# Performance work log

Measured on AMD Instinct MI355X. Metric: run time of the kernel, lower is better.

## Reference

```python
import jax, jax.numpy as jnp
import numpy as np

B, L, H, V = 256, 4096, 64, 64
LN_EPS = 1e-5


def setup_inputs() -> dict:
    key = jax.random.key(0)
    ks = jax.random.split(key, 12)
    s = 1.0 / np.sqrt(H)
    return {
        "seq": jax.random.randint(ks[0], (B, L), 0, V),
        "embed_W": jax.random.normal(ks[1], (V, H), jnp.float32),
        "ff_w1": jax.random.normal(ks[2], (H, 2 * H), jnp.float32) * s,
        "ff_b1": jnp.zeros((2 * H,), jnp.float32),
        "ff_w2": jax.random.normal(ks[3], (2 * H, H), jnp.float32) * s,
        "ff_b2": jnp.zeros((H,), jnp.float32),
        "ln_w": jnp.ones((H,), jnp.float32),
        "ln_b": jnp.zeros((H,), jnp.float32),
        "read_w": jax.random.normal(ks[4], (H, H), jnp.float32) * s,
        "read_b": jnp.zeros((H,), jnp.float32),
        "out_w": jax.random.normal(ks[5], (H, V), jnp.float32) * s,
        "out_b": jnp.zeros((V,), jnp.float32),
    }


def _layer_norm(x, w, b):
    mu = jnp.mean(x, axis=-1, keepdims=True)
    var = jnp.mean(jnp.square(x - mu), axis=-1, keepdims=True)
    return (x - mu) * jax.lax.rsqrt(var + LN_EPS) * w + b


def reference(seq, embed_W, ff_w1, ff_b1, ff_w2, ff_b2, ln_w, ln_b,
              read_w, read_b, out_w, out_b):
    h = embed_W[seq]  # (B, L, H)
    ff = jax.nn.relu(h @ ff_w1 + ff_b1) @ ff_w2 + ff_b2
    h = _layer_norm(h + ff, ln_w, ln_b)

    def step(M, k):  # M: (B,H,H), k: (B,H)
        v_pred = jnp.einsum('bij,bj->bi', M, k)
        denom = jnp.sum(k * k, axis=-1, keepdims=True) + 1e-6
        dv = k - v_pred / denom
        M = M + dv[:, :, None] * k[:, None, :]  # rank-1 delta write
        return M, None

    ks = jnp.swapaxes(h[:, :-1, :], 0, 1)  # (L-1, B, H)
    M0 = jnp.zeros((h.shape[0], h.shape[-1], h.shape[-1]), h.dtype)
    M, _ = jax.lax.scan(step, M0, ks)

    q = h[:, -1, :]
    ctx = jnp.einsum('bij,bj->bi', M, q)
    return (ctx @ read_w + read_b) @ out_w + out_b  # (B, V)
```

## Files before the change

kernel.cpp:

```cpp
#include <hip/hip_runtime.h>
#include <hip/hip_bf16.h>

#define LN_EPS 1e-5f

static __device__ __forceinline__ float readlane_f(float v, int lane) {
    return __int_as_float(__builtin_amdgcn_readlane(__float_as_int(v), lane));
}

__global__ __launch_bounds__(64) void build_keys(
    const float* __restrict__ embed,
    const float* __restrict__ w1,
    const float* __restrict__ b1,
    const float* __restrict__ w2,
    const float* __restrict__ b2,
    const float* __restrict__ lnw,
    const float* __restrict__ lnb,
    float* __restrict__ keytab)
{
    const int v = blockIdx.x, lane = threadIdx.x;
    __shared__ float se[64];
    __shared__ float sh[128];
    se[lane] = embed[v * 64 + lane];
    __syncthreads();
    float h0 = b1[lane];
    float h1 = b1[lane + 64];
    #pragma unroll 8
    for (int i = 0; i < 64; ++i) {
        float e = se[i];
        h0 = fmaf(e, w1[i * 128 + lane], h0);
        h1 = fmaf(e, w1[i * 128 + lane + 64], h1);
    }
    sh[lane]      = fmaxf(h0, 0.f);
    sh[lane + 64] = fmaxf(h1, 0.f);
    __syncthreads();
    float acc = b2[lane];
    #pragma unroll 8
    for (int j = 0; j < 128; ++j)
        acc = fmaf(sh[j], w2[j * 64 + lane], acc);
    float pre = se[lane] + acc;
    float sum = pre;
    #pragma unroll
    for (int off = 32; off >= 1; off >>= 1) sum += __shfl_xor(sum, off, 64);
    float mu  = sum * (1.f / 64.f);
    float dev = pre - mu;
    float sq  = dev * dev;
    #pragma unroll
    for (int off = 32; off >= 1; off >>= 1) sq += __shfl_xor(sq, off, 64);
    float var = sq * (1.f / 64.f);
    float key = dev * (1.f / sqrtf(var + LN_EPS)) * lnw[lane] + lnb[lane];
    keytab[v * 64 + lane] = key;
}

__global__ __launch_bounds__(64) void build_tables(
    const float* __restrict__ keytab,
    const float* __restrict__ read_w,
    const float* __restrict__ read_b,
    const float* __restrict__ out_w,
    const float* __restrict__ out_b,
    float* __restrict__ Gg,
    float* __restrict__ Ghat,
    float* __restrict__ Wc,
    float* __restrict__ biasv)
{
    const int w = blockIdx.x, lane = threadIdx.x;
    __shared__ float sk[64 * 65];
    __shared__ float srw[64];
    #pragma unroll 8
    for (int r = 0; r < 64; ++r) sk[r * 65 + lane] = keytab[r * 64 + lane];
    srw[lane] = read_w[w * 64 + lane];
    __syncthreads();
    float g = 0.f;
    #pragma unroll 8
    for (int i = 0; i < 64; ++i)
        g = fmaf(sk[w * 65 + i], sk[lane * 65 + i], g);
    float gww  = readlane_f(g, w);
    float beta = 1.f / (gww + 1e-6f);
    Gg[w * 64 + lane]   = g;
    Ghat[w * 64 + lane] = beta * g;
    float acc = 0.f;
    #pragma unroll 8
    for (int j = 0; j < 64; ++j)
        acc = fmaf(srw[j], out_w[j * 64 + lane], acc);
    Wc[w * 64 + lane] = acc;
    if (w == 0) {
        float bacc = out_b[lane];
        #pragma unroll 8
        for (int j = 0; j < 64; ++j)
            bacc = fmaf(read_b[j], out_w[j * 64 + lane], bacc);
        biasv[lane] = bacc;
    }
}

__global__ __launch_bounds__(64) void delta_scan(
    const int*   __restrict__ seq,
    const float* __restrict__ Gg,
    const float* __restrict__ Ghat,
    const float* __restrict__ keytab,
    const float* __restrict__ Wc,
    const float* __restrict__ biasv,
    float* __restrict__ out)
{
    const int lane = threadIdx.x;
    const int b    = blockIdx.x;
    __shared__ float sG[64 * 64];
    __shared__ float sC[64];
    __shared__ float sCtx[64];
    #pragma unroll 8
    for (int r = 0; r < 64; ++r) sG[r * 64 + lane] = Ghat[r * 64 + lane];
    const int* seqb = seq + (size_t)b * 4096;
    const int wq = seqb[4095];
    float d = Gg[wq * 64 + lane];
    __syncthreads();

    float c = 0.f, s1 = 0.f, gh1 = 0.f;
    int vcur = seqb[64 * 63 + lane];
    float q_[9];
    #pragma unroll
    for (int m = 0; m < 9; ++m) {
        int w = __builtin_amdgcn_readlane(vcur, 62 - m);
        q_[m] = sG[w * 64 + lane];
    }
    for (int blk = 64; blk >= 0; --blk) {
        int vnext = (blk > 0) ? seqb[(blk - 1) * 63 + lane] : vcur;
        #pragma unroll
        for (int j = 62; j >= 0; --j) {
            const int slot = (62 - j) % 9;
            int   w0 = __builtin_amdgcn_readlane(vcur, j);
            float p  = readlane_f(d, w0);
            float g  = readlane_f(gh1, w0);
            float s0 = fmaf(-s1, g, p);
            d = fmaf(-s1, gh1, d);
            c += (lane == w0) ? s0 : 0.f;
            float rown = q_[slot];
            int jl = j - 9;
            int wpre = (jl >= 0) ? __builtin_amdgcn_readlane(vcur, jl)
                                 : __builtin_amdgcn_readlane(vnext, jl + 63);
            q_[slot] = sG[wpre * 64 + lane];
            s1 = s0; gh1 = rown;
        }
        vcur = vnext;
    }

    sC[lane] = c;
    __syncthreads();
    float ctx = 0.f;
    #pragma unroll 8
    for (int v = 0; v < 64; ++v)
        ctx = fmaf(sC[v], keytab[v * 64 + lane], ctx);
    sCtx[lane] = ctx;
    __syncthreads();
    float o = biasv[lane];
    #pragma unroll 8
    for (int i = 0; i < 64; ++i)
        o = fmaf(sCtx[i], Wc[i * 64 + lane], o);
    out[(size_t)b * 64 + lane] = o;
}

extern "C" void kernel_launch(void* const* d_in, const int* in_sizes, int n_in,
                              void* d_out, int out_size, void* d_ws, size_t ws_size,
                              hipStream_t stream) {
    const int*   seq    = (const int*)d_in[0];
    const float* embed  = (const float*)d_in[1];
    const float* ff_w1  = (const float*)d_in[2];
    const float* ff_b1  = (const float*)d_in[3];
    const float* ff_w2  = (const float*)d_in[4];
    const float* ff_b2  = (const float*)d_in[5];
    const float* ln_w   = (const float*)d_in[6];
    const float* ln_b   = (const float*)d_in[7];
    const float* read_w = (const float*)d_in[8];
    const float* read_b = (const float*)d_in[9];
    const float* out_w  = (const float*)d_in[10];
    const float* out_b  = (const float*)d_in[11];
    float* out = (float*)d_out;

    float* wsf    = (float*)d_ws;
    float* keytab = wsf;
    float* Gg     = wsf + 4096;
    float* Ghat   = wsf + 8192;
    float* Wc     = wsf + 12288;
    float* biasv  = wsf + 16384;

    build_keys<<<64, 64, 0, stream>>>(embed, ff_w1, ff_b1, ff_w2, ff_b2, ln_w, ln_b, keytab);
    build_tables<<<64, 64, 0, stream>>>(keytab, read_w, read_b, out_w, out_b,
                                        Gg, Ghat, Wc, biasv);
    delta_scan<<<256, 64, 0, stream>>>(seq, Gg, Ghat, keytab, Wc, biasv, out);
}
```

Before: 197.9 us.

## Simplify delta-scan recurrence, deepen prefetch, batch coefficient accumulation via LDS atomics

Reformulates the backward scan recurrence so each step needs one readlane and one FMA on d, using a negated normalized Gram table instead of the two-term update with s1/gh1. The prefetch ring of Gram rows grows from 9 to 21 slots, and the word indices are cached in registers. Per-step coefficients are collected with v_writelane into a register and accumulated once per block through an LDS atomicAdd, which replaces the per-step per-lane select-add. The aim is a shorter serial dependency chain per step, at the cost of more VGPRs and inline asm.

```diff
diff --git a/kernel.cpp b/kernel.cpp
--- a/kernel.cpp
+++ b/kernel.cpp
@@ -5,6 +5,11 @@
 
 static __device__ __forceinline__ float readlane_f(float v, int lane) {
     return __int_as_float(__builtin_amdgcn_readlane(__float_as_int(v), lane));
+}
+static __device__ __forceinline__ void writelane_f(int& dst, float val, int lane_imm) {
+    asm volatile("v_writelane_b32 %0, %1, %2"
+                 : "+v"(dst)
+                 : "s"(__float_as_int(val)), "i"(lane_imm));
 }
 
 __global__ __launch_bounds__(64) void build_keys(
@@ -58,7 +63,7 @@
     const float* __restrict__ out_w,
     const float* __restrict__ out_b,
     float* __restrict__ Gg,
-    float* __restrict__ Ghat,
+    float* __restrict__ GhatN,
     float* __restrict__ Wc,
     float* __restrict__ biasv)
 {
@@ -75,8 +80,8 @@
         g = fmaf(sk[w * 65 + i], sk[lane * 65 + i], g);
     float gww  = readlane_f(g, w);
     float beta = 1.f / (gww + 1e-6f);
-    Gg[w * 64 + lane]   = g;
-    Ghat[w * 64 + lane] = beta * g;
+    Gg[w * 64 + lane]    = g;
+    GhatN[w * 64 + lane] = -(beta * g);
     float acc = 0.f;
     #pragma unroll 8
     for (int j = 0; j < 64; ++j)
@@ -94,7 +99,7 @@
 __global__ __launch_bounds__(64) void delta_scan(
     const int*   __restrict__ seq,
     const float* __restrict__ Gg,
-    const float* __restrict__ Ghat,
+    const float* __restrict__ GhatN,
     const float* __restrict__ keytab,
     const float* __restrict__ Wc,
     const float* __restrict__ biasv,
@@ -103,50 +108,51 @@
     const int lane = threadIdx.x;
     const int b    = blockIdx.x;
     __shared__ float sG[64 * 64];
-    __shared__ float sC[64];
+    __shared__ float sc[64];
     __shared__ float sCtx[64];
     #pragma unroll 8
-    for (int r = 0; r < 64; ++r) sG[r * 64 + lane] = Ghat[r * 64 + lane];
+    for (int r = 0; r < 64; ++r) sG[r * 64 + lane] = GhatN[r * 64 + lane];
+    sc[lane] = 0.f;
     const int* seqb = seq + (size_t)b * 4096;
-    const int wq = seqb[4095];
-    float d = Gg[wq * 64 + lane];
+    float d = Gg[seqb[4095] * 64 + lane];
     __syncthreads();
 
-    float c = 0.f, s1 = 0.f, gh1 = 0.f;
+    int vS = 0;
     int vcur = seqb[64 * 63 + lane];
-    float q_[9];
+    int   wq[21];
+    float q_[21];
     #pragma unroll
-    for (int m = 0; m < 9; ++m) {
-        int w = __builtin_amdgcn_readlane(vcur, 62 - m);
-        q_[m] = sG[w * 64 + lane];
+    for (int s = 0; s < 21; ++s) {
+        wq[s] = __builtin_amdgcn_readlane(vcur, 62 - s);
+        q_[s] = sG[wq[s] * 64 + lane];
     }
+
+    #pragma unroll 1
     for (int blk = 64; blk >= 0; --blk) {
         int vnext = (blk > 0) ? seqb[(blk - 1) * 63 + lane] : vcur;
         #pragma unroll
         for (int j = 62; j >= 0; --j) {
-            const int slot = (62 - j) % 9;
-            int   w0 = __builtin_amdgcn_readlane(vcur, j);
+            const int slot = (62 - j) % 21;
+            const int jl   = j - 21;
+            int   w0 = wq[slot];
             float p  = readlane_f(d, w0);
-            float g  = readlane_f(gh1, w0);
-            float s0 = fmaf(-s1, g, p);
-            d = fmaf(-s1, gh1, d);
-            c += (lane == w0) ? s0 : 0.f;
-            float rown = q_[slot];
-            int jl = j - 9;
-            int wpre = (jl >= 0) ? __builtin_amdgcn_readlane(vcur, jl)
-                                 : __builtin_amdgcn_readlane(vnext, jl + 63);
-            q_[slot] = sG[wpre * 64 + lane];
-            s1 = s0; gh1 = rown;
+            d = fmaf(p, q_[slot], d);
+            writelane_f(vS, p, j);
+            int wn = (jl >= 0) ? __builtin_amdgcn_readlane(vcur, jl)
+                               : __builtin_amdgcn_readlane(vnext, jl + 63);
+            wq[slot] = wn;
+            q_[slot] = sG[wn * 64 + lane];
         }
+        atomicAdd(&sc[vcur & 63], __int_as_float(vS));
+        vS = 0;
         vcur = vnext;
     }
+    __syncthreads();
 
-    sC[lane] = c;
-    __syncthreads();
     float ctx = 0.f;
     #pragma unroll 8
     for (int v = 0; v < 64; ++v)
-        ctx = fmaf(sC[v], keytab[v * 64 + lane], ctx);
+        ctx = fmaf(sc[v], keytab[v * 64 + lane], ctx);
     sCtx[lane] = ctx;
     __syncthreads();
     float o = biasv[lane];
@@ -176,12 +182,12 @@
     float* wsf    = (float*)d_ws;
     float* keytab = wsf;
     float* Gg     = wsf + 4096;
-    float* Ghat   = wsf + 8192;
+    float* GhatN  = wsf + 8192;
     float* Wc     = wsf + 12288;
     float* biasv  = wsf + 16384;
 
     build_keys<<<64, 64, 0, stream>>>(embed, ff_w1, ff_b1, ff_w2, ff_b2, ln_w, ln_b, keytab);
     build_tables<<<64, 64, 0, stream>>>(keytab, read_w, read_b, out_w, out_b,
-                                        Gg, Ghat, Wc, biasv);
-    delta_scan<<<256, 64, 0, stream>>>(seq, Gg, Ghat, keytab, Wc, biasv, out);
+                                        Gg, GhatN, Wc, biasv);
+    delta_scan<<<256, 64, 0, stream>>>(seq, Gg, GhatN, keytab, Wc, biasv, out);
 }
```

Measured after the change: 168.3 us. -15.0%, faster.
